# Performance work log

Hardware: AMD Instinct MI355X
Metric: run time of the kernel (lower is better)

Reference implementation:

```python
import jax, jax.numpy as jnp
import numpy as np

K = 9  # ATSS top-k candidates per GT


def cxcywh_to_xyxy(b):
    cx, cy, w, h = b[..., 0], b[..., 1], b[..., 2], b[..., 3]
    return jnp.stack([cx - 0.5 * w, cy - 0.5 * h, cx + 0.5 * w, cy + 0.5 * h], axis=-1)


def elementwise_iou(a, b):
    # a, b: [..., 4] xyxy, broadcastable
    lt = jnp.maximum(a[..., :2], b[..., :2])
    rb = jnp.minimum(a[..., 2:], b[..., 2:])
    wh = jnp.clip(rb - lt, 0.0)
    inter = wh[..., 0] * wh[..., 1]
    area_a = (a[..., 2] - a[..., 0]) * (a[..., 3] - a[..., 1])
    area_b = (b[..., 2] - b[..., 0]) * (b[..., 3] - b[..., 1])
    return inter / (area_a + area_b - inter)


def setup_inputs() -> dict:
    key = jax.random.key(0)
    k1, k2 = jax.random.split(key)
    pred_boxes = jax.random.uniform(k1, (16, 30000, 4), dtype=jnp.float32)
    gt_boxes = jax.random.uniform(k2, (16, 64, 4), dtype=jnp.float32)
    return {"pred_boxes": pred_boxes, "gt_boxes": gt_boxes}


def reference(pred_boxes, gt_boxes):
    # pred_boxes: [B, N, 4] cxcywh; gt_boxes: [B, G, 4] cxcywh
    G = gt_boxes.shape[1]

    def per_image(pred, gt):
        # center-distance matrix [G, N] (the cdist in the original)
        diff = gt[:, None, :2] - pred[None, :, :2]
        dist = jnp.sqrt(jnp.sum(diff * diff, axis=-1))
        # k smallest distances per GT
        _, k_idx = jax.lax.top_k(-dist, K)          # [G, K]
        k_boxes = pred[k_idx]                        # [G, K, 4]
        gt_xyxy = cxcywh_to_xyxy(gt)                 # [G, 4]
        kb_xyxy = cxcywh_to_xyxy(k_boxes)            # [G, K, 4]
        ious = elementwise_iou(gt_xyxy[:, None, :], kb_xyxy)  # [G, K]
        # adaptive threshold: mean + std (torch.std is unbiased -> ddof=1)
        thr = jnp.mean(ious, axis=1, keepdims=True) + jnp.std(ious, axis=1, ddof=1, keepdims=True)
        cx, cy = k_boxes[..., 0], k_boxes[..., 1]
        inside = ((gt_xyxy[:, None, 0] <= cx) & (cx <= gt_xyxy[:, None, 2]) &
                  (gt_xyxy[:, None, 1] <= cy) & (cy <= gt_xyxy[:, None, 3]))
        mask = (ious >= thr) & inside                # [G, K]
        # padded index representation (original returns ragged lists):
        pred_idx = jnp.where(mask, k_idx, -1)
        gt_idx = jnp.where(mask, jnp.arange(G, dtype=jnp.int64)[:, None], -1)
        return pred_idx, gt_idx, mask, ious

    return jax.vmap(per_image)(pred_boxes, gt_boxes)
```

## Files before the change

### kernel.cpp

```cpp
#include <hip/hip_runtime.h>
#include <stdint.h>

typedef unsigned long long u64;

#define KCAND 9
#define BATCH 16
#define NPRED 30000
#define NGT   64
#define TPB   256
#define UNR   8
#define NT    15
#define INITKEY 0x7F800000FFFFFFFFULL
#define FINF __uint_as_float(0x7F800000u)

__global__ __launch_bounds__(256) void compact_xy(
    const float* __restrict__ pred, float2* __restrict__ xy)
{
    int e = blockIdx.x * 256 + threadIdx.x;
    if (e < BATCH * NPRED) {
        float4 p = ((const float4*)pred)[e];
        xy[e] = make_float2(p.x, p.y);
    }
}

template <int S2, bool MASK>
__device__ __forceinline__ void load_d2(const float2* __restrict__ xyb, int i0,
                                        float gcx, float gcy, float (&d2)[UNR]) {
#pragma unroll
    for (int j = 0; j < UNR; ++j) {
        const int i = i0 + j * 64;
        const bool v = !MASK || (i < NPRED);
        float2 p = xyb[(v ? i : 0) * S2];
        float dx = __fsub_rn(gcx, p.x);
        float dy = __fsub_rn(gcy, p.y);
        float d  = __fadd_rn(__fmul_rn(dx, dx), __fmul_rn(dy, dy));
        d2[j] = v ? d : FINF;
    }
}

template <int S2>
__global__ __launch_bounds__(TPB, 4) void atss_kernel(
    const float2* __restrict__ xy,
    const float*  __restrict__ pred,
    const float*  __restrict__ gt,
    float* __restrict__ out)
{
#pragma clang fp contract(off)
    const int tid  = threadIdx.x;
    const int lane = tid & 63;
    const int wvid = tid >> 6;

    const int b = (blockIdx.x & 7) + 8 * (blockIdx.x >> 9);
    const int g = (blockIdx.x >> 3) & 63;
    const int w = b * NGT + g;

    const float4 gtb = ((const float4*)gt)[w];
    const float gcx = gtb.x, gcy = gtb.y;
    const float2* xyb   = xy + (size_t)b * NPRED * S2;
    const float4* pred4 = (const float4*)pred + (size_t)b * NPRED;

    const int ibase0 = wvid * (64 * UNR) + lane;

    float lmin = FINF;
    for (int t = 0; t < NT - 1; ++t) {
        float d2[UNR];
        load_d2<S2, false>(xyb, t * (TPB * UNR) + ibase0, gcx, gcy, d2);
#pragma unroll
        for (int j = 0; j < UNR; ++j) lmin = fminf(lmin, d2[j]);
    }
    {
        float d2[UNR];
        load_d2<S2, true>(xyb, (NT - 1) * (TPB * UNR) + ibase0, gcx, gcy, d2);
#pragma unroll
        for (int j = 0; j < UNR; ++j) lmin = fminf(lmin, d2[j]);
    }

    {
        float x = lmin;
#pragma unroll
        for (int k = 2; k <= 64; k <<= 1) {
#pragma unroll
            for (int j = k >> 1; j >= 1; j >>= 1) {
                float o = __shfl_xor(x, j, 64);
                bool keepmin = (((lane & k) == 0) == ((lane & j) == 0));
                x = keepmin ? fminf(x, o) : fmaxf(x, o);
            }
        }
        lmin = x;
    }
    float Tf = __uint_as_float((unsigned)__builtin_amdgcn_readlane(
                                   (int)__float_as_uint(lmin), 8));

    u64 t0=INITKEY,t1=INITKEY,t2=INITKEY,t3=INITKEY,t4=INITKEY,
        t5=INITKEY,t6=INITKEY,t7=INITKEY,t8=INITKEY;

#define SW(T) { bool c_ = x < (T); u64 lo_ = c_ ? x : (T); u64 hi_ = c_ ? (T) : x; (T) = lo_; x = hi_; }
#define SWAP9 SW(t0) SW(t1) SW(t2) SW(t3) SW(t4) SW(t5) SW(t6) SW(t7) SW(t8)

#define PROCESS(I0) { \
    float dmin = d2[0]; \
    _Pragma("unroll") \
    for (int j = 1; j < UNR; ++j) dmin = fminf(dmin, d2[j]); \
    if (__ballot(dmin <= Tf) != 0ULL) { \
        _Pragma("unroll") \
        for (int j = 0; j < UNR; ++j) { \
            u64 pend = __ballot(d2[j] <= Tf); \
            while (pend) { \
                const int src = __ffsll(pend) - 1; \
                pend &= pend - 1; \
                const unsigned kd = (unsigned)__builtin_amdgcn_readlane( \
                                        (int)__float_as_uint(d2[j]), src); \
                const unsigned ki = (unsigned)((I0) - lane + j * 64 + src); \
                u64 key = ((u64)kd << 32) | ki; \
                if (key < t8) { \
                    u64 x = key; SWAP9; \
                    Tf = fminf(Tf, __uint_as_float((unsigned)(t8 >> 32))); \
                    pend &= __ballot(d2[j] <= Tf); \
                } \
            } \
        } \
    } }

    for (int t = 0; t < NT - 1; ++t) {
        const int i0 = t * (TPB * UNR) + ibase0;
        float d2[UNR];
        load_d2<S2, false>(xyb, i0, gcx, gcy, d2);
        PROCESS(i0)
    }
    {
        const int i0 = (NT - 1) * (TPB * UNR) + ibase0;
        float d2[UNR];
        load_d2<S2, true>(xyb, i0, gcx, gcy, d2);
        PROCESS(i0)
    }

    __shared__ u64 smem[4 * KCAND];
    if (lane == 0) {
        u64* s = smem + wvid * KCAND;
        s[0]=t0; s[1]=t1; s[2]=t2; s[3]=t3; s[4]=t4;
        s[5]=t5; s[6]=t6; s[7]=t7; s[8]=t8;
    }
    __syncthreads();

    if (wvid != 0) return;

    u64 cand = (lane < 4 * KCAND) ? smem[lane] : INITKEY;
    const float cd = __uint_as_float((unsigned)(cand >> 32));
    t0=INITKEY;t1=INITKEY;t2=INITKEY;t3=INITKEY;t4=INITKEY;
    t5=INITKEY;t6=INITKEY;t7=INITKEY;t8=INITKEY;
    Tf = FINF;
    {
        u64 pend = __ballot(cd < FINF);
        while (pend) {
            const int src = __ffsll(pend) - 1;
            pend &= pend - 1;
            const unsigned kd = (unsigned)__builtin_amdgcn_readlane(
                                    (int)(unsigned)(cand >> 32), src);
            const unsigned ki = (unsigned)__builtin_amdgcn_readlane(
                                    (int)(unsigned)cand, src);
            u64 key = ((u64)kd << 32) | ki;
            if (key < t8) {
                u64 x = key; SWAP9;
                Tf = fminf(Tf, __uint_as_float((unsigned)(t8 >> 32)));
                pend &= __ballot(cd <= Tf);
            }
        }
    }

    u64 fin = t0;
    if (lane == 1) fin = t1;
    if (lane == 2) fin = t2;
    if (lane == 3) fin = t3;
    if (lane == 4) fin = t4;
    if (lane == 5) fin = t5;
    if (lane == 6) fin = t6;
    if (lane == 7) fin = t7;
    if (lane == 8) fin = t8;

    const bool active = (lane < KCAND);
    const unsigned idx = active ? (unsigned)(fin & 0xffffffffu) : 0u;

    float4 pb = pred4[idx];

    float gx1 = gcx - 0.5f * gtb.z, gy1 = gcy - 0.5f * gtb.w;
    float gx2 = gcx + 0.5f * gtb.z, gy2 = gcy + 0.5f * gtb.w;
    float kx1 = pb.x - 0.5f * pb.z, ky1 = pb.y - 0.5f * pb.w;
    float kx2 = pb.x + 0.5f * pb.z, ky2 = pb.y + 0.5f * pb.w;

    float ltx = fmaxf(gx1, kx1), lty = fmaxf(gy1, ky1);
    float rbx = fminf(gx2, kx2), rby = fminf(gy2, ky2);
    float wvd = fmaxf(rbx - ltx, 0.0f);
    float hvd = fmaxf(rby - lty, 0.0f);
    float inter  = wvd * hvd;
    float area_a = (gx2 - gx1) * (gy2 - gy1);
    float area_b = (kx2 - kx1) * (ky2 - ky1);
    float iou = inter / ((area_a + area_b) - inter);

    float v = active ? iou : 0.0f;
    float s = v;
#pragma unroll
    for (int m = 1; m < 64; m <<= 1) s += __shfl_xor(s, m, 64);
    float mean = s / 9.0f;

    float dev = active ? (iou - mean) : 0.0f;
    float ss = dev * dev;
#pragma unroll
    for (int m = 1; m < 64; m <<= 1) ss += __shfl_xor(ss, m, 64);
    float stdv = sqrtf(ss / 8.0f);
    float thr = mean + stdv;

    bool inside = (gx1 <= pb.x) && (pb.x <= gx2) &&
                  (gy1 <= pb.y) && (pb.y <= gy2);
    bool maskk = (iou >= thr) && inside;

    if (active) {
        const size_t chunk = (size_t)BATCH * NGT * KCAND;
        const size_t o = (size_t)w * KCAND + lane;
        out[0 * chunk + o] = maskk ? (float)idx : -1.0f;
        out[1 * chunk + o] = maskk ? (float)g   : -1.0f;
        out[2 * chunk + o] = maskk ? 1.0f : 0.0f;
        out[3 * chunk + o] = iou;
    }
#undef PROCESS
#undef SWAP9
#undef SW
}

extern "C" void kernel_launch(void* const* d_in, const int* in_sizes, int n_in,
                              void* d_out, int out_size, void* d_ws, size_t ws_size,
                              hipStream_t stream) {
    const float* pred = (const float*)d_in[0];
    const float* gtb  = (const float*)d_in[1];
    float* out = (float*)d_out;

    const size_t need = (size_t)BATCH * NPRED * sizeof(float2);
    if (ws_size >= need) {
        float2* xyc = (float2*)d_ws;
        compact_xy<<<(BATCH * NPRED + 255) / 256, 256, 0, stream>>>(pred, xyc);
        atss_kernel<1><<<BATCH * NGT, TPB, 0, stream>>>(xyc, pred, gtb, out);
    } else {
        atss_kernel<2><<<BATCH * NGT, TPB, 0, stream>>>(
            (const float2*)pred, pred, gtb, out);
    }
}
```

Measured before the change: 99.70 us.

## Split ATSS top-k into subsample threshold, survivor collection, and finalize kernels

Computes a per-GT distance upper bound from an every-8th subsample, then scans all predictions once per image against all 64 GTs at once. Candidates under the bound are compacted into a per-GT survivor list with atomics. A finalize kernel selects the top 9 from the survivors, falling back to a full scan if the list overflows. This removes the two full per-GT passes over 30k predictions, at the cost of extra launches, a memset, atomics and a larger workspace.

```diff
diff --git a/kernel.cpp b/kernel.cpp
--- a/kernel.cpp
+++ b/kernel.cpp
@@ -7,162 +7,192 @@
 #define BATCH 16
 #define NPRED 30000
 #define NGT   64
-#define TPB   256
-#define UNR   8
-#define NT    15
+#define SUBN  3750
+#define CHUNK 1024
+#define NCH   30
+#define CAP   1024
 #define INITKEY 0x7F800000FFFFFFFFULL
 #define FINF __uint_as_float(0x7F800000u)
 
-__global__ __launch_bounds__(256) void compact_xy(
-    const float* __restrict__ pred, float2* __restrict__ xy)
+__device__ __forceinline__ float rl_f(float v, int l) {
+    return __uint_as_float((unsigned)__builtin_amdgcn_readlane((int)__float_as_uint(v), l));
+}
+
+__global__ __launch_bounds__(256) void compact_k(
+    const float* __restrict__ pred, float2* __restrict__ xy, float2* __restrict__ sub)
 {
     int e = blockIdx.x * 256 + threadIdx.x;
     if (e < BATCH * NPRED) {
         float4 p = ((const float4*)pred)[e];
         xy[e] = make_float2(p.x, p.y);
-    }
-}
-
-template <int S2, bool MASK>
-__device__ __forceinline__ void load_d2(const float2* __restrict__ xyb, int i0,
-                                        float gcx, float gcy, float (&d2)[UNR]) {
-#pragma unroll
-    for (int j = 0; j < UNR; ++j) {
-        const int i = i0 + j * 64;
-        const bool v = !MASK || (i < NPRED);
-        float2 p = xyb[(v ? i : 0) * S2];
+        int b = e / NPRED;
+        int i = e - b * NPRED;
+        if ((i & 7) == 0) sub[b * SUBN + (i >> 3)] = make_float2(p.x, p.y);
+    }
+}
+
+__global__ __launch_bounds__(256) void thresh_k(
+    const float2* __restrict__ sub, const float* __restrict__ gt, float* __restrict__ T)
+{
+#pragma clang fp contract(off)
+    const int lane = threadIdx.x & 63;
+    const int wvid = threadIdx.x >> 6;
+    const int row  = blockIdx.x * 4 + wvid;
+    const int b    = row >> 6;
+
+    const float gcx = gt[row * 4 + 0], gcy = gt[row * 4 + 1];
+    const float2* sb = sub + b * SUBN;
+
+    float lmin = FINF;
+#pragma unroll 4
+    for (int k = lane; k < SUBN; k += 64) {
+        float2 p = sb[k];
         float dx = __fsub_rn(gcx, p.x);
         float dy = __fsub_rn(gcy, p.y);
         float d  = __fadd_rn(__fmul_rn(dx, dx), __fmul_rn(dy, dy));
-        d2[j] = v ? d : FINF;
-    }
-}
-
-template <int S2>
-__global__ __launch_bounds__(TPB, 4) void atss_kernel(
-    const float2* __restrict__ xy,
-    const float*  __restrict__ pred,
-    const float*  __restrict__ gt,
+        lmin = fminf(lmin, d);
+    }
+    float x = lmin;
+#pragma unroll
+    for (int k = 2; k <= 64; k <<= 1) {
+#pragma unroll
+        for (int j = k >> 1; j >= 1; j >>= 1) {
+            float o = __shfl_xor(x, j, 64);
+            bool keepmin = (((lane & k) == 0) == ((lane & j) == 0));
+            x = keepmin ? fminf(x, o) : fmaxf(x, o);
+        }
+    }
+    if (lane == 8) T[row] = x;
+}
+
+__global__ __launch_bounds__(256, 4) void collect_k(
+    const float2* __restrict__ xy, const float* __restrict__ gt,
+    const float* __restrict__ T, unsigned* __restrict__ cnt, u64* __restrict__ surv)
+{
+#pragma clang fp contract(off)
+    const int lane = threadIdx.x & 63;
+    const int wvid = threadIdx.x >> 6;
+    const int b = blockIdx.x & 15;
+    const int c = blockIdx.x >> 4;
+    const int rowbase = b * NGT;
+
+    float gx_v = gt[(rowbase + lane) * 4 + 0];
+    float gy_v = gt[(rowbase + lane) * 4 + 1];
+    float Tv   = T[rowbase + lane];
+
+    const int i0 = c * CHUNK + wvid * 256 + lane * 4;
+    const float4* xb4 = (const float4*)(xy + (size_t)b * NPRED);
+    const int f0 = i0 >> 1;
+    float4 A = xb4[f0 < NPRED / 2 ? f0 : NPRED / 2 - 1];
+    float4 Bq = xb4[f0 + 1 < NPRED / 2 ? f0 + 1 : NPRED / 2 - 1];
+    float ex[4] = {A.x, A.z, Bq.x, Bq.z};
+    float ey[4] = {A.y, A.w, Bq.y, Bq.w};
+#pragma unroll
+    for (int j = 0; j < 4; ++j)
+        if (i0 + j >= NPRED) { ex[j] = FINF; ey[j] = FINF; }
+
+    const u64 below = ((u64)1 << lane) - 1;
+
+    for (int g = 0; g < NGT; ++g) {
+        const float gcx = rl_f(gx_v, g);
+        const float gcy = rl_f(gy_v, g);
+        const float Tg  = rl_f(Tv, g);
+
+        float d2[4]; bool p[4];
+#pragma unroll
+        for (int j = 0; j < 4; ++j) {
+            float dx = __fsub_rn(gcx, ex[j]);
+            float dy = __fsub_rn(gcy, ey[j]);
+            d2[j] = __fadd_rn(__fmul_rn(dx, dx), __fmul_rn(dy, dy));
+            p[j] = d2[j] <= Tg;
+        }
+        if (__ballot(p[0] | p[1] | p[2] | p[3]) == 0ULL) continue;
+
+        u64 b0 = __ballot(p[0]), b1 = __ballot(p[1]), b2 = __ballot(p[2]), b3 = __ballot(p[3]);
+        int tot = __popcll(b0) + __popcll(b1) + __popcll(b2) + __popcll(b3);
+        unsigned base = 0;
+        if (lane == 0) base = atomicAdd(&cnt[rowbase + g], (unsigned)tot);
+        base = (unsigned)__shfl((int)base, 0, 64);
+
+        int c0 = __popcll(b0), c1 = c0 + __popcll(b1), c2 = c1 + __popcll(b2);
+        int pos[4];
+        pos[0] = __popcll(b0 & below);
+        pos[1] = c0 + __popcll(b1 & below);
+        pos[2] = c1 + __popcll(b2 & below);
+        pos[3] = c2 + __popcll(b3 & below);
+
+        u64* sr = surv + (size_t)(rowbase + g) * CAP;
+#pragma unroll
+        for (int j = 0; j < 4; ++j) {
+            if (p[j]) {
+                unsigned q = base + (unsigned)pos[j];
+                if (q < CAP)
+                    sr[q] = ((u64)__float_as_uint(d2[j]) << 32) | (unsigned)(i0 + j);
+            }
+        }
+    }
+}
+
+#define SW(Tq) { bool c_ = x < (Tq); u64 lo_ = c_ ? x : (Tq); u64 hi_ = c_ ? (Tq) : x; (Tq) = lo_; x = hi_; }
+#define SWAP9 SW(t0) SW(t1) SW(t2) SW(t3) SW(t4) SW(t5) SW(t6) SW(t7) SW(t8)
+
+__global__ __launch_bounds__(256) void finalize_k(
+    const float2* __restrict__ xy, const float* __restrict__ pred,
+    const float* __restrict__ gt, const float* __restrict__ T,
+    const unsigned* __restrict__ cnt, const u64* __restrict__ surv,
     float* __restrict__ out)
 {
 #pragma clang fp contract(off)
-    const int tid  = threadIdx.x;
-    const int lane = tid & 63;
-    const int wvid = tid >> 6;
-
-    const int b = (blockIdx.x & 7) + 8 * (blockIdx.x >> 9);
-    const int g = (blockIdx.x >> 3) & 63;
-    const int w = b * NGT + g;
-
-    const float4 gtb = ((const float4*)gt)[w];
+    const int lane = threadIdx.x & 63;
+    const int wvid = threadIdx.x >> 6;
+    const int row  = blockIdx.x * 4 + wvid;
+    const int b = row >> 6, g = row & 63;
+
+    const float4 gtb = ((const float4*)gt)[row];
     const float gcx = gtb.x, gcy = gtb.y;
-    const float2* xyb   = xy + (size_t)b * NPRED * S2;
     const float4* pred4 = (const float4*)pred + (size_t)b * NPRED;
-
-    const int ibase0 = wvid * (64 * UNR) + lane;
-
-    float lmin = FINF;
-    for (int t = 0; t < NT - 1; ++t) {
-        float d2[UNR];
-        load_d2<S2, false>(xyb, t * (TPB * UNR) + ibase0, gcx, gcy, d2);
-#pragma unroll
-        for (int j = 0; j < UNR; ++j) lmin = fminf(lmin, d2[j]);
-    }
-    {
-        float d2[UNR];
-        load_d2<S2, true>(xyb, (NT - 1) * (TPB * UNR) + ibase0, gcx, gcy, d2);
-#pragma unroll
-        for (int j = 0; j < UNR; ++j) lmin = fminf(lmin, d2[j]);
-    }
-
-    {
-        float x = lmin;
-#pragma unroll
-        for (int k = 2; k <= 64; k <<= 1) {
-#pragma unroll
-            for (int j = k >> 1; j >= 1; j >>= 1) {
-                float o = __shfl_xor(x, j, 64);
-                bool keepmin = (((lane & k) == 0) == ((lane & j) == 0));
-                x = keepmin ? fminf(x, o) : fmaxf(x, o);
-            }
-        }
-        lmin = x;
-    }
-    float Tf = __uint_as_float((unsigned)__builtin_amdgcn_readlane(
-                                   (int)__float_as_uint(lmin), 8));
 
     u64 t0=INITKEY,t1=INITKEY,t2=INITKEY,t3=INITKEY,t4=INITKEY,
         t5=INITKEY,t6=INITKEY,t7=INITKEY,t8=INITKEY;
 
-#define SW(T) { bool c_ = x < (T); u64 lo_ = c_ ? x : (T); u64 hi_ = c_ ? (T) : x; (T) = lo_; x = hi_; }
-#define SWAP9 SW(t0) SW(t1) SW(t2) SW(t3) SW(t4) SW(t5) SW(t6) SW(t7) SW(t8)
-
-#define PROCESS(I0) { \
-    float dmin = d2[0]; \
-    _Pragma("unroll") \
-    for (int j = 1; j < UNR; ++j) dmin = fminf(dmin, d2[j]); \
-    if (__ballot(dmin <= Tf) != 0ULL) { \
-        _Pragma("unroll") \
-        for (int j = 0; j < UNR; ++j) { \
-            u64 pend = __ballot(d2[j] <= Tf); \
-            while (pend) { \
-                const int src = __ffsll(pend) - 1; \
-                pend &= pend - 1; \
-                const unsigned kd = (unsigned)__builtin_amdgcn_readlane( \
-                                        (int)__float_as_uint(d2[j]), src); \
-                const unsigned ki = (unsigned)((I0) - lane + j * 64 + src); \
-                u64 key = ((u64)kd << 32) | ki; \
-                if (key < t8) { \
-                    u64 x = key; SWAP9; \
-                    Tf = fminf(Tf, __uint_as_float((unsigned)(t8 >> 32))); \
-                    pend &= __ballot(d2[j] <= Tf); \
-                } \
-            } \
-        } \
-    } }
-
-    for (int t = 0; t < NT - 1; ++t) {
-        const int i0 = t * (TPB * UNR) + ibase0;
-        float d2[UNR];
-        load_d2<S2, false>(xyb, i0, gcx, gcy, d2);
-        PROCESS(i0)
-    }
-    {
-        const int i0 = (NT - 1) * (TPB * UNR) + ibase0;
-        float d2[UNR];
-        load_d2<S2, true>(xyb, i0, gcx, gcy, d2);
-        PROCESS(i0)
-    }
-
-    __shared__ u64 smem[4 * KCAND];
-    if (lane == 0) {
-        u64* s = smem + wvid * KCAND;
-        s[0]=t0; s[1]=t1; s[2]=t2; s[3]=t3; s[4]=t4;
-        s[5]=t5; s[6]=t6; s[7]=t7; s[8]=t8;
-    }
-    __syncthreads();
-
-    if (wvid != 0) return;
-
-    u64 cand = (lane < 4 * KCAND) ? smem[lane] : INITKEY;
-    const float cd = __uint_as_float((unsigned)(cand >> 32));
-    t0=INITKEY;t1=INITKEY;t2=INITKEY;t3=INITKEY;t4=INITKEY;
-    t5=INITKEY;t6=INITKEY;t7=INITKEY;t8=INITKEY;
-    Tf = FINF;
-    {
-        u64 pend = __ballot(cd < FINF);
-        while (pend) {
-            const int src = __ffsll(pend) - 1;
-            pend &= pend - 1;
-            const unsigned kd = (unsigned)__builtin_amdgcn_readlane(
-                                    (int)(unsigned)(cand >> 32), src);
-            const unsigned ki = (unsigned)__builtin_amdgcn_readlane(
-                                    (int)(unsigned)cand, src);
-            u64 key = ((u64)kd << 32) | ki;
-            if (key < t8) {
-                u64 x = key; SWAP9;
-                Tf = fminf(Tf, __uint_as_float((unsigned)(t8 >> 32)));
-                pend &= __ballot(cd <= Tf);
+    const unsigned n = cnt[row];
+    if (n <= (unsigned)CAP) {
+        const u64* sr = surv + (size_t)row * CAP;
+        for (unsigned bs = 0; bs < n; bs += 64) {
+            u64 cand = (bs + lane < n) ? sr[bs + lane] : INITKEY;
+            u64 pend = __ballot(cand < t8);
+            while (pend) {
+                const int src = __ffsll(pend) - 1;
+                pend &= pend - 1;
+                const unsigned kd = (unsigned)__builtin_amdgcn_readlane((int)(unsigned)(cand >> 32), src);
+                const unsigned ki = (unsigned)__builtin_amdgcn_readlane((int)(unsigned)cand, src);
+                u64 key = ((u64)kd << 32) | ki;
+                if (key < t8) {
+                    u64 x = key; SWAP9;
+                    pend &= __ballot(cand < t8);
+                }
+            }
+        }
+    } else {
+        float Tf = T[row];
+        const float2* xb = xy + (size_t)b * NPRED;
+        for (int k = lane; k < NPRED; k += 64) {
+            float2 p = xb[k];
+            float dx = __fsub_rn(gcx, p.x);
+            float dy = __fsub_rn(gcy, p.y);
+            float d2 = __fadd_rn(__fmul_rn(dx, dx), __fmul_rn(dy, dy));
+            u64 pend = __ballot(d2 <= Tf);
+            while (pend) {
+                const int src = __ffsll(pend) - 1;
+                pend &= pend - 1;
+                const unsigned kd = (unsigned)__builtin_amdgcn_readlane((int)__float_as_uint(d2), src);
+                const unsigned ki = (unsigned)(k - lane + src);
+                u64 key = ((u64)kd << 32) | ki;
+                if (key < t8) {
+                    u64 x = key; SWAP9;
+                    Tf = fminf(Tf, __uint_as_float((unsigned)(t8 >> 32)));
+                    pend &= __ballot(d2 <= Tf);
+                }
             }
         }
     }
@@ -215,16 +245,139 @@
 
     if (active) {
         const size_t chunk = (size_t)BATCH * NGT * KCAND;
+        const size_t o = (size_t)row * KCAND + lane;
+        out[0 * chunk + o] = maskk ? (float)idx : -1.0f;
+        out[1 * chunk + o] = maskk ? (float)g   : -1.0f;
+        out[2 * chunk + o] = maskk ? 1.0f : 0.0f;
+        out[3 * chunk + o] = iou;
+    }
+}
+
+__global__ __launch_bounds__(256, 4) void atss_fb(
+    const float* __restrict__ pred, const float* __restrict__ gt, float* __restrict__ out)
+{
+#pragma clang fp contract(off)
+    const int lane = threadIdx.x & 63;
+    const int wvid = threadIdx.x >> 6;
+    const int b = (blockIdx.x & 7) + 8 * (blockIdx.x >> 9);
+    const int g = (blockIdx.x >> 3) & 63;
+    const int w = b * NGT + g;
+
+    const float4 gtb = ((const float4*)gt)[w];
+    const float gcx = gtb.x, gcy = gtb.y;
+    const float4* pred4 = (const float4*)pred + (size_t)b * NPRED;
+
+    float lmin = FINF;
+    for (int k = wvid * 64 + lane; k < NPRED; k += 256) {
+        float4 p = pred4[k];
+        float dx = __fsub_rn(gcx, p.x);
+        float dy = __fsub_rn(gcy, p.y);
+        lmin = fminf(lmin, __fadd_rn(__fmul_rn(dx, dx), __fmul_rn(dy, dy)));
+    }
+    {
+        float x = lmin;
+#pragma unroll
+        for (int k = 2; k <= 64; k <<= 1)
+#pragma unroll
+            for (int j = k >> 1; j >= 1; j >>= 1) {
+                float o = __shfl_xor(x, j, 64);
+                bool keepmin = (((lane & k) == 0) == ((lane & j) == 0));
+                x = keepmin ? fminf(x, o) : fmaxf(x, o);
+            }
+        lmin = x;
+    }
+    float Tf = rl_f(lmin, 8);
+
+    u64 t0=INITKEY,t1=INITKEY,t2=INITKEY,t3=INITKEY,t4=INITKEY,
+        t5=INITKEY,t6=INITKEY,t7=INITKEY,t8=INITKEY;
+    for (int k = wvid * 64 + lane; k < NPRED; k += 256) {
+        float4 p = pred4[k];
+        float dx = __fsub_rn(gcx, p.x);
+        float dy = __fsub_rn(gcy, p.y);
+        float d2 = __fadd_rn(__fmul_rn(dx, dx), __fmul_rn(dy, dy));
+        u64 pend = __ballot(d2 <= Tf);
+        while (pend) {
+            const int src = __ffsll(pend) - 1;
+            pend &= pend - 1;
+            const unsigned kd = (unsigned)__builtin_amdgcn_readlane((int)__float_as_uint(d2), src);
+            const unsigned ki = (unsigned)(k - lane + src);
+            u64 key = ((u64)kd << 32) | ki;
+            if (key < t8) {
+                u64 x = key; SWAP9;
+                Tf = fminf(Tf, __uint_as_float((unsigned)(t8 >> 32)));
+                pend &= __ballot(d2 <= Tf);
+            }
+        }
+    }
+
+    __shared__ u64 smem[4 * KCAND];
+    if (lane == 0) {
+        u64* sm = smem + wvid * KCAND;
+        sm[0]=t0; sm[1]=t1; sm[2]=t2; sm[3]=t3; sm[4]=t4;
+        sm[5]=t5; sm[6]=t6; sm[7]=t7; sm[8]=t8;
+    }
+    __syncthreads();
+    if (wvid != 0) return;
+
+    u64 cand = (lane < 4 * KCAND) ? smem[lane] : INITKEY;
+    t0=INITKEY;t1=INITKEY;t2=INITKEY;t3=INITKEY;t4=INITKEY;
+    t5=INITKEY;t6=INITKEY;t7=INITKEY;t8=INITKEY;
+    {
+        u64 pend = __ballot(cand < INITKEY);
+        while (pend) {
+            const int src = __ffsll(pend) - 1;
+            pend &= pend - 1;
+            const unsigned kd = (unsigned)__builtin_amdgcn_readlane((int)(unsigned)(cand >> 32), src);
+            const unsigned ki = (unsigned)__builtin_amdgcn_readlane((int)(unsigned)cand, src);
+            u64 key = ((u64)kd << 32) | ki;
+            if (key < t8) { u64 x = key; SWAP9; pend &= __ballot(cand < t8); }
+        }
+    }
+    u64 fin = t0;
+    if (lane == 1) fin = t1;
+    if (lane == 2) fin = t2;
+    if (lane == 3) fin = t3;
+    if (lane == 4) fin = t4;
+    if (lane == 5) fin = t5;
+    if (lane == 6) fin = t6;
+    if (lane == 7) fin = t7;
+    if (lane == 8) fin = t8;
+
+    const bool active = (lane < KCAND);
+    const unsigned idx = active ? (unsigned)(fin & 0xffffffffu) : 0u;
+    float4 pb = pred4[idx];
+    float gx1 = gcx - 0.5f * gtb.z, gy1 = gcy - 0.5f * gtb.w;
+    float gx2 = gcx + 0.5f * gtb.z, gy2 = gcy + 0.5f * gtb.w;
+    float kx1 = pb.x - 0.5f * pb.z, ky1 = pb.y - 0.5f * pb.w;
+    float kx2 = pb.x + 0.5f * pb.z, ky2 = pb.y + 0.5f * pb.w;
+    float ltx = fmaxf(gx1, kx1), lty = fmaxf(gy1, ky1);
+    float rbx = fminf(gx2, kx2), rby = fminf(gy2, ky2);
+    float wvd = fmaxf(rbx - ltx, 0.0f), hvd = fmaxf(rby - lty, 0.0f);
+    float inter  = wvd * hvd;
+    float area_a = (gx2 - gx1) * (gy2 - gy1);
+    float area_b = (kx2 - kx1) * (ky2 - ky1);
+    float iou = inter / ((area_a + area_b) - inter);
+    float v = active ? iou : 0.0f, s = v;
+#pragma unroll
+    for (int m = 1; m < 64; m <<= 1) s += __shfl_xor(s, m, 64);
+    float mean = s / 9.0f;
+    float dev = active ? (iou - mean) : 0.0f, ss = dev * dev;
+#pragma unroll
+    for (int m = 1; m < 64; m <<= 1) ss += __shfl_xor(ss, m, 64);
+    float thr = mean + sqrtf(ss / 8.0f);
+    bool inside = (gx1 <= pb.x) && (pb.x <= gx2) && (gy1 <= pb.y) && (pb.y <= gy2);
+    bool maskk = (iou >= thr) && inside;
+    if (active) {
+        const size_t chunk = (size_t)BATCH * NGT * KCAND;
         const size_t o = (size_t)w * KCAND + lane;
         out[0 * chunk + o] = maskk ? (float)idx : -1.0f;
         out[1 * chunk + o] = maskk ? (float)g   : -1.0f;
         out[2 * chunk + o] = maskk ? 1.0f : 0.0f;
         out[3 * chunk + o] = iou;
     }
-#undef PROCESS
+}
 #undef SWAP9
 #undef SW
-}
 
 extern "C" void kernel_launch(void* const* d_in, const int* in_sizes, int n_in,
                               void* d_out, int out_size, void* d_ws, size_t ws_size,
@@ -233,13 +386,27 @@
     const float* gtb  = (const float*)d_in[1];
     float* out = (float*)d_out;
 
-    const size_t need = (size_t)BATCH * NPRED * sizeof(float2);
+    const size_t off_xy   = 0;
+    const size_t off_sub  = off_xy  + (size_t)BATCH * NPRED * sizeof(float2);
+    const size_t off_T    = off_sub + (size_t)BATCH * SUBN  * sizeof(float2);
+    const size_t off_cnt  = off_T   + (size_t)BATCH * NGT * sizeof(float);
+    const size_t off_surv = off_cnt + (size_t)BATCH * NGT * sizeof(unsigned);
+    const size_t need     = off_surv + (size_t)BATCH * NGT * CAP * sizeof(u64);
+
     if (ws_size >= need) {
-        float2* xyc = (float2*)d_ws;
-        compact_xy<<<(BATCH * NPRED + 255) / 256, 256, 0, stream>>>(pred, xyc);
-        atss_kernel<1><<<BATCH * NGT, TPB, 0, stream>>>(xyc, pred, gtb, out);
+        char* ws = (char*)d_ws;
+        float2*   xy   = (float2*)(ws + off_xy);
+        float2*   sub  = (float2*)(ws + off_sub);
+        float*    T    = (float*)(ws + off_T);
+        unsigned* cnt  = (unsigned*)(ws + off_cnt);
+        u64*      surv = (u64*)(ws + off_surv);
+
+        compact_k<<<(BATCH * NPRED + 255) / 256, 256, 0, stream>>>(pred, xy, sub);
+        hipMemsetAsync(cnt, 0, (size_t)BATCH * NGT * sizeof(unsigned), stream);
+        thresh_k<<<BATCH * NGT / 4, 256, 0, stream>>>(sub, gtb, T);
+        collect_k<<<BATCH * NCH, 256, 0, stream>>>(xy, gtb, T, cnt, surv);
+        finalize_k<<<BATCH * NGT / 4, 256, 0, stream>>>(xy, pred, gtb, T, cnt, surv, out);
     } else {
-        atss_kernel<2><<<BATCH * NGT, TPB, 0, stream>>>(
-            (const float2*)pred, pred, gtb, out);
-    }
-}
+        atss_fb<<<BATCH * NGT, 256, 0, stream>>>(pred, gtb, out);
+    }
+}
```

Result: slower. 148.7 us (+49.1%).
